# Performance work log

Measured on AMD Instinct MI355X. Metric: run time of the kernel, lower is better.

Reference implementation:

```python
import jax, jax.numpy as jnp
import numpy as np

# gen_dx_bx([-30,30,0.15], [-15,15,0.15])
DX = jnp.array([0.15, 0.15], dtype=jnp.float32)
BX = jnp.array([-29.925, -14.925], dtype=jnp.float32)


def _pairwise_dist(a, b):
    # torch.cdist p=2: [Na,2] x [Nb,2] -> [Na,Nb]
    return jnp.sqrt(jnp.sum((a[:, None, :] - b[None, :, :]) ** 2, axis=-1))


def _single(match, position, semantic, pts, ins, typ):
    # match [M,M] (M=N+1 with dustbin), position [N,2], semantic [C,N],
    # pts [G,2], ins [G] int, typ [G] int. Assumes mask is all-ones (set in setup_inputs).
    N = position.shape[0]
    M = match.shape[0]
    G = pts.shape[0]
    C = semantic.shape[0]

    pos = position * DX + BX                      # grid -> meters
    cd = _pairwise_dist(pos, pts)                 # [N,G]
    nearest = cd.argmin(-1).astype(jnp.int32)     # [N]
    cdist_mean = jnp.mean(cd.min(-1))             # mean of per-pred nearest-GT distance
    dist_map = _pairwise_dist(pos, pos)           # [N,N]
    nmax = nearest.max()

    # precompute, for every gt index g, whether any pred maps to it and the
    # closest such pred (torch: idx_pred_next[cdist[idx_pred_next, g].argmin()])
    assign = nearest[:, None] == jnp.arange(G, dtype=jnp.int32)[None, :]  # [N,G]
    exists_g = assign.any(0)                                              # [G]
    best_pred_g = jnp.where(assign, cd, jnp.inf).argmin(0).astype(jnp.int32)  # [G]

    def walk(start_gt):
        # greedy forward walk along gt indices; replicates the python while-loop,
        # including torch's negative-index wrap (idx % G) for idx_gt_next = -1.
        def cond(st):
            return ~st[2]

        def body(st):
            idx, steps, done, res = st
            is_end = idx >= nmax
            g_next_raw = jnp.where(is_end, jnp.int32(-1), idx + 1)
            g_next = jnp.mod(g_next_raw, G)
            ex = (~is_end) & exists_g[g_next]  # nearest==-1 never holds in torch
            same = ins[jnp.mod(idx, G)] == ins[g_next]
            matched = ex & same
            stop = matched | (~same) | (steps >= G + 2)  # safety bound
            res_new = jnp.where(matched, best_pred_g[g_next], jnp.int32(-1))
            return (g_next_raw, steps + jnp.int32(1), stop, res_new)

        st = (start_gt, jnp.int32(0), jnp.bool_(False), jnp.int32(-1))
        return jax.lax.while_loop(cond, body, st)[3]

    next_pred = jax.vmap(walk)(nearest)  # [N], -1 means no match (dustbin later)

    # build match_gt [M,M]
    A = jnp.zeros((M, M), dtype=match.dtype)
    valid = next_pred >= 0
    cols = jnp.where(valid, next_pred, 0)
    A = A.at[jnp.arange(N), cols].max(valid.astype(match.dtype))

    # resolve columns matched by multiple rows: keep the row closest in dist_map
    Acols = A[:, :N]
    col_sum = Acols.sum(0)
    dist_pad = jnp.concatenate([dist_map, jnp.full((1, N), jnp.inf, dist_map.dtype)], 0)  # [M,N]
    keep = jnp.where(Acols > 0, dist_pad, jnp.inf).argmin(0)  # [N]
    onehot = (jnp.arange(M)[:, None] == keep[None, :]).astype(match.dtype)
    Acols = jnp.where(col_sum[None, :] > 1, onehot, Acols)
    A = A.at[:, :N].set(Acols)

    # unmatched pred rows -> dustbin column; unmatched pred cols -> dustbin row
    row_sum = A[:N].sum(1)
    A = A.at[:N, M - 1].set(jnp.where(row_sum == 0, 1.0, A[:N, M - 1]))
    col_sum2 = A[:, :N].sum(0)
    A = A.at[M - 1, :N].set(jnp.where(col_sum2 == 0, 1.0, A[M - 1, :N]))

    # semantic gt: one-hot of the type of each pred's nearest gt point
    cls = typ[nearest]  # [N]
    semantic_gt = (jnp.arange(C)[:, None] == cls[None, :]).astype(semantic.dtype)  # [C,N]

    # NLL match loss (torch transposes then feeds NLLLoss: loss = -match[j, target[j]])
    tgt_b = A.argmax(0)  # per-column gt row
    tgt_f = A.argmax(1)  # per-row gt col
    j = jnp.arange(M - 1)
    loss_b = -jnp.mean(match[j, tgt_b[: M - 1]])
    loss_f = -jnp.mean(match[j, tgt_f[: M - 1]])
    match_loss = 0.5 * (loss_f + loss_b)

    sem_loss = -jnp.mean(semantic[semantic_gt.argmax(0), jnp.arange(N)])
    return cdist_mean, match_loss, sem_loss, A, semantic_gt


def setup_inputs() -> dict:
    key = jax.random.key(0)
    ks = jax.random.split(key, 5)
    B, N, G, C, NI = 4, 2048, 1024, 3, 32
    # log-probability score matrix with dustbin (Sinkhorn-style output)
    matches = jax.nn.log_softmax(jax.random.normal(ks[0], (B, N + 1, N + 1), jnp.float32), axis=-1)
    # predicted vertex grid coords on the 400x200 BEV grid
    positions = jax.random.uniform(ks[1], (B, N, 2), jnp.float32) * jnp.array([400.0, 200.0], jnp.float32)
    semantics = jax.nn.log_softmax(jax.random.normal(ks[2], (B, C, N), jnp.float32), axis=1)
    masks = jnp.ones((B, N, 1), jnp.float32)
    # gt points in meters within the BEV range
    gt_pts = (jax.random.uniform(ks[3], (B, G, 2), jnp.float32) - 0.5) * jnp.array([60.0, 30.0], jnp.float32)
    # sorted instance ids -> contiguous runs like the original per-instance list build
    gt_ins = jnp.sort(jax.random.randint(ks[4], (B, G), 0, NI), axis=-1).astype(jnp.int32)
    gt_type = (gt_ins % C).astype(jnp.int32)
    return {"matches": matches, "positions": positions, "semantics": semantics,
            "masks": masks, "gt_pts": gt_pts, "gt_ins": gt_ins, "gt_type": gt_type}


def reference(matches, positions, semantics, masks, gt_pts, gt_ins, gt_type):
    cm, ml, sl, mg, sg = jax.vmap(_single)(matches, positions, semantics, gt_pts, gt_ins, gt_type)
    # reduction='mean'
    return jnp.mean(cm), jnp.mean(ml), jnp.mean(sl), mg, sg
```

## Files before the change

kernel.cpp:

```cpp
#include <hip/hip_runtime.h>
#include <math.h>

#define BB 4
#define NN 2048
#define GG 1024
#define CC 3
#define MM 2049
#define SP 8
#define CH (GG / SP)

typedef unsigned long long u64;
#define KEY_EMPTY 0xFFFFFFFFFFFFFFFFULL

struct Ws {
  u64   near_key[BB * NN];
  u64   best_key[BB * GG];
  u64   keep_key[BB * NN];
  int   nearest[BB * NN];
  int   next_pred[BB * NN];
  int   col_cnt[BB * NN];
  int   nmax[BB];
  float cdist_sum[BB];
  float sem_sum[BB];
  float lossf_sum[BB];
  float lossb_sum[BB];
};

__device__ __forceinline__ float posx(float p) { return __fadd_rn(__fmul_rn(p, 0.15f), -29.925f); }
__device__ __forceinline__ float posy(float p) { return __fadd_rn(__fmul_rn(p, 0.15f), -14.925f); }
__device__ __forceinline__ float pdist(float ax, float ay, float bx, float by) {
  float dx = __fsub_rn(ax, bx);
  float dy = __fsub_rn(ay, by);
  return __fsqrt_rn(__fadd_rn(__fmul_rn(dx, dx), __fmul_rn(dy, dy)));
}
__device__ __forceinline__ u64 pack_key(float d, int i) {
  return ((u64)__float_as_uint(d) << 32) | (unsigned int)i;
}


__global__ void k_init(Ws* ws) {
  int t = blockIdx.x * blockDim.x + threadIdx.x;
  if (t < BB * NN) {
    ws->near_key[t] = KEY_EMPTY;
    ws->keep_key[t] = KEY_EMPTY;
    ws->col_cnt[t] = 0;
  }
  if (t < BB * GG) ws->best_key[t] = KEY_EMPTY;
  if (t < BB) {
    ws->nmax[t] = 0;
    ws->cdist_sum[t] = 0.f;
    ws->sem_sum[t] = 0.f;
    ws->lossf_sum[t] = 0.f;
    ws->lossb_sum[t] = 0.f;
  }
}

__global__ __launch_bounds__(256) void k_near1(const float* __restrict__ positions,
                                               const float* __restrict__ gt_pts, Ws* ws) {
  __shared__ float spts[CH * 2];
  const int cpb = NN / 256;
  int b = blockIdx.x / (cpb * SP);
  int r = blockIdx.x % (cpb * SP);
  int i = (r / SP) * 256 + threadIdx.x;
  int g0 = (r % SP) * CH;

  spts[threadIdx.x] = gt_pts[b * GG * 2 + g0 * 2 + threadIdx.x];
  __syncthreads();

  float px = posx(positions[(size_t)(b * NN + i) * 2 + 0]);
  float py = posy(positions[(size_t)(b * NN + i) * 2 + 1]);

  float dmin = INFINITY;
  int gmin = 0;
  #pragma unroll 4
  for (int g = 0; g < CH; ++g) {
    float d = pdist(px, py, spts[2 * g], spts[2 * g + 1]);
    if (d < dmin) { dmin = d; gmin = g; }
  }
  atomicMin(&ws->near_key[b * NN + i], pack_key(dmin, g0 + gmin));
}

__global__ __launch_bounds__(64) void k_near2(const int* __restrict__ gt_type,
                                              const float* __restrict__ semantics,
                                              Ws* ws, float* __restrict__ out) {
  int b = blockIdx.x >> 5;
  int i = (blockIdx.x & 31) * 64 + threadIdx.x;

  u64 key = ws->near_key[b * NN + i];
  float dmin = __uint_as_float((unsigned int)(key >> 32));
  int g = (int)(key & 0xFFFFFFFFULL);

  ws->nearest[b * NN + i] = g;
  atomicMin(&ws->best_key[b * GG + g], pack_key(dmin, i));

  int cls = gt_type[b * GG + g];
  float* sg = out + 3 + (size_t)BB * MM * MM;
  sg[(size_t)b * CC * NN + 0 * NN + i] = (cls == 0) ? 1.f : 0.f;
  sg[(size_t)b * CC * NN + 1 * NN + i] = (cls == 1) ? 1.f : 0.f;
  sg[(size_t)b * CC * NN + 2 * NN + i] = (cls == 2) ? 1.f : 0.f;
  float sem = semantics[(size_t)b * CC * NN + (size_t)cls * NN + i];

  float v = dmin;
  #pragma unroll
  for (int o = 32; o > 0; o >>= 1) v += __shfl_down(v, o, 64);
  if (threadIdx.x == 0) atomicAdd(&ws->cdist_sum[b], v);

  v = sem;
  #pragma unroll
  for (int o = 32; o > 0; o >>= 1) v += __shfl_down(v, o, 64);
  if (threadIdx.x == 0) atomicAdd(&ws->sem_sum[b], v);

  int m = g;
  #pragma unroll
  for (int o = 32; o > 0; o >>= 1) m = max(m, __shfl_down(m, o, 64));
  if (threadIdx.x == 0) atomicMax(&ws->nmax[b], m);
}

__global__ __launch_bounds__(64) void k_walk(const int* __restrict__ gt_ins,
                                             const float* __restrict__ positions, Ws* ws) {
  __shared__ int sins[GG];
  __shared__ int sbest[GG];
  int b = blockIdx.x >> 5;
  int i = (blockIdx.x & 31) * 64 + threadIdx.x;

  {
    const int4* src = reinterpret_cast<const int4*>(gt_ins + b * GG);
    int4* dst = reinterpret_cast<int4*>(sins);
    for (int t = threadIdx.x; t < GG / 4; t += 64) dst[t] = src[t];
    const u64* bk = ws->best_key + b * GG;
    for (int t = threadIdx.x; t < GG; t += 64) {
      u64 k = bk[t];
      sbest[t] = (k == KEY_EMPTY) ? -1 : (int)(k & 0xFFFFFFFFULL);
    }
  }
  __syncthreads();

  int nmax = ws->nmax[b];
  int idx = ws->nearest[b * NN + i];
  int steps = 0, res = -1;
  while (true) {
    bool is_end = idx >= nmax;
    int gnr = is_end ? -1 : idx + 1;
    int gn = gnr & (GG - 1);
    bool ex = (!is_end) && (sbest[gn] >= 0);
    bool same = sins[idx & (GG - 1)] == sins[gn];
    bool matched = ex && same;
    res = matched ? sbest[gn] : -1;
    bool stop = matched || (!same) || (steps >= GG + 2);
    idx = gnr;
    ++steps;
    if (stop) break;
  }
  ws->next_pred[b * NN + i] = res;
  if (res >= 0) {
    atomicAdd(&ws->col_cnt[b * NN + res], 1);
    const float* pb = positions + (size_t)b * NN * 2;
    float d = pdist(posx(pb[2 * i]), posy(pb[2 * i + 1]),
                    posx(pb[2 * res]), posy(pb[2 * res + 1]));
    atomicMin(&ws->keep_key[b * NN + res], pack_key(d, i));
  }
}

__global__ __launch_bounds__(64) void k_post(const float* __restrict__ matches,
                                             Ws* ws, float* __restrict__ out) {
  int b = blockIdx.x >> 5;
  int i = (blockIdx.x & 31) * 64 + threadIdx.x;

  float* A = out + 3 + (size_t)b * MM * MM;

  int j = ws->next_pred[b * NN + i];
  bool surv = (j >= 0) && ((int)(ws->keep_key[b * NN + j] & 0xFFFFFFFFULL) == i);
  if (surv) A[(size_t)i * MM + j] = 1.0f;
  else      A[(size_t)i * MM + (MM - 1)] = 1.0f;

  int cnt = ws->col_cnt[b * NN + i];
  if (cnt == 0) A[(size_t)(MM - 1) * MM + i] = 1.0f;

  int tf = surv ? j : (MM - 1);
  float vf = matches[(size_t)b * MM * MM + (size_t)i * MM + tf];
  int tb = (cnt > 0) ? (int)(ws->keep_key[b * NN + i] & 0xFFFFFFFFULL) : (MM - 1);
  float vb = matches[(size_t)b * MM * MM + (size_t)i * MM + tb];

  float v = vf;
  #pragma unroll
  for (int o = 32; o > 0; o >>= 1) v += __shfl_down(v, o, 64);
  if (threadIdx.x == 0) atomicAdd(&ws->lossf_sum[b], v);

  v = vb;
  #pragma unroll
  for (int o = 32; o > 0; o >>= 1) v += __shfl_down(v, o, 64);
  if (threadIdx.x == 0) atomicAdd(&ws->lossb_sum[b], v);
}

__global__ void k_final(Ws* ws, float* __restrict__ out) {
  if (threadIdx.x == 0 && blockIdx.x == 0) {
    float cm = 0.f, ml = 0.f, sl = 0.f;
    for (int b = 0; b < BB; ++b) {
      cm += ws->cdist_sum[b] / (float)NN;
      float lf = -(ws->lossf_sum[b] / (float)(MM - 1));
      float lb = -(ws->lossb_sum[b] / (float)(MM - 1));
      ml += 0.5f * (lf + lb);
      sl += -(ws->sem_sum[b] / (float)NN);
    }
    out[0] = cm / (float)BB;
    out[1] = ml / (float)BB;
    out[2] = sl / (float)BB;
  }
}

extern "C" void kernel_launch(void* const* d_in, const int* in_sizes, int n_in,
                              void* d_out, int out_size, void* d_ws, size_t ws_size,
                              hipStream_t stream) {
  (void)in_sizes; (void)n_in; (void)ws_size;
  const float* matches   = (const float*)d_in[0];
  const float* positions = (const float*)d_in[1];
  const float* semantics = (const float*)d_in[2];
  const float* gt_pts    = (const float*)d_in[4];
  const int*   gt_ins    = (const int*)d_in[5];
  const int*   gt_type   = (const int*)d_in[6];
  float* out = (float*)d_out;
  Ws* ws = (Ws*)d_ws;

  hipMemsetAsync(d_out, 0, (size_t)out_size * sizeof(float), stream);
  k_init<<<(BB * NN + 255) / 256, 256, 0, stream>>>(ws);
  k_near1<<<BB * (NN / 256) * SP, 256, 0, stream>>>(positions, gt_pts, ws);
  k_near2<<<BB * (NN / 64), 64, 0, stream>>>(gt_type, semantics, ws, out);
  k_walk<<<BB * (NN / 64), 64, 0, stream>>>(gt_ins, positions, ws);
  k_post<<<BB * (NN / 64), 64, 0, stream>>>(matches, ws, out);
  k_final<<<1, 64, 0, stream>>>(ws, out);
}
```

Before: 150.8 us.

## Fuse all stages into one cooperative kernel with grid syncs

```diff
diff --git a/kernel.cpp b/kernel.cpp
--- a/kernel.cpp
+++ b/kernel.cpp
@@ -1,5 +1,8 @@
 #include <hip/hip_runtime.h>
+#include <hip/hip_cooperative_groups.h>
 #include <math.h>
+
+namespace cg = cooperative_groups;
 
 #define BB 4
 #define NN 2048
@@ -8,6 +11,8 @@
 #define MM 2049
 #define SP 8
 #define CH (GG / SP)
+#define NBLK 256
+#define NTHR 256
 
 typedef unsigned long long u64;
 #define KEY_EMPTY 0xFFFFFFFFFFFFFFFFULL
@@ -37,163 +42,171 @@
   return ((u64)__float_as_uint(d) << 32) | (unsigned int)i;
 }
 
-
-__global__ void k_init(Ws* ws) {
-  int t = blockIdx.x * blockDim.x + threadIdx.x;
-  if (t < BB * NN) {
-    ws->near_key[t] = KEY_EMPTY;
-    ws->keep_key[t] = KEY_EMPTY;
-    ws->col_cnt[t] = 0;
-  }
-  if (t < BB * GG) ws->best_key[t] = KEY_EMPTY;
-  if (t < BB) {
-    ws->nmax[t] = 0;
-    ws->cdist_sum[t] = 0.f;
-    ws->sem_sum[t] = 0.f;
-    ws->lossf_sum[t] = 0.f;
-    ws->lossb_sum[t] = 0.f;
-  }
-}
-
-__global__ __launch_bounds__(256) void k_near1(const float* __restrict__ positions,
-                                               const float* __restrict__ gt_pts, Ws* ws) {
-  __shared__ float spts[CH * 2];
-  const int cpb = NN / 256;
-  int b = blockIdx.x / (cpb * SP);
-  int r = blockIdx.x % (cpb * SP);
-  int i = (r / SP) * 256 + threadIdx.x;
-  int g0 = (r % SP) * CH;
-
-  spts[threadIdx.x] = gt_pts[b * GG * 2 + g0 * 2 + threadIdx.x];
-  __syncthreads();
-
-  float px = posx(positions[(size_t)(b * NN + i) * 2 + 0]);
-  float py = posy(positions[(size_t)(b * NN + i) * 2 + 1]);
-
-  float dmin = INFINITY;
-  int gmin = 0;
-  #pragma unroll 4
-  for (int g = 0; g < CH; ++g) {
-    float d = pdist(px, py, spts[2 * g], spts[2 * g + 1]);
-    if (d < dmin) { dmin = d; gmin = g; }
-  }
-  atomicMin(&ws->near_key[b * NN + i], pack_key(dmin, g0 + gmin));
-}
-
-__global__ __launch_bounds__(64) void k_near2(const int* __restrict__ gt_type,
+__global__ __launch_bounds__(NTHR) void k_all(const float* __restrict__ matches,
+                                              const float* __restrict__ positions,
                                               const float* __restrict__ semantics,
-                                              Ws* ws, float* __restrict__ out) {
-  int b = blockIdx.x >> 5;
-  int i = (blockIdx.x & 31) * 64 + threadIdx.x;
-
-  u64 key = ws->near_key[b * NN + i];
-  float dmin = __uint_as_float((unsigned int)(key >> 32));
-  int g = (int)(key & 0xFFFFFFFFULL);
-
-  ws->nearest[b * NN + i] = g;
-  atomicMin(&ws->best_key[b * GG + g], pack_key(dmin, i));
-
-  int cls = gt_type[b * GG + g];
-  float* sg = out + 3 + (size_t)BB * MM * MM;
-  sg[(size_t)b * CC * NN + 0 * NN + i] = (cls == 0) ? 1.f : 0.f;
-  sg[(size_t)b * CC * NN + 1 * NN + i] = (cls == 1) ? 1.f : 0.f;
-  sg[(size_t)b * CC * NN + 2 * NN + i] = (cls == 2) ? 1.f : 0.f;
-  float sem = semantics[(size_t)b * CC * NN + (size_t)cls * NN + i];
-
-  float v = dmin;
-  #pragma unroll
-  for (int o = 32; o > 0; o >>= 1) v += __shfl_down(v, o, 64);
-  if (threadIdx.x == 0) atomicAdd(&ws->cdist_sum[b], v);
-
-  v = sem;
-  #pragma unroll
-  for (int o = 32; o > 0; o >>= 1) v += __shfl_down(v, o, 64);
-  if (threadIdx.x == 0) atomicAdd(&ws->sem_sum[b], v);
-
-  int m = g;
-  #pragma unroll
-  for (int o = 32; o > 0; o >>= 1) m = max(m, __shfl_down(m, o, 64));
-  if (threadIdx.x == 0) atomicMax(&ws->nmax[b], m);
-}
-
-__global__ __launch_bounds__(64) void k_walk(const int* __restrict__ gt_ins,
-                                             const float* __restrict__ positions, Ws* ws) {
-  __shared__ int sins[GG];
-  __shared__ int sbest[GG];
-  int b = blockIdx.x >> 5;
-  int i = (blockIdx.x & 31) * 64 + threadIdx.x;
+                                              const float* __restrict__ gt_pts,
+                                              const int* __restrict__ gt_ins,
+                                              const int* __restrict__ gt_type,
+                                              Ws* ws, float* __restrict__ out, int out_size) {
+  cg::grid_group grid = cg::this_grid();
+  __shared__ int smem[2 * GG];
+  const int bid = blockIdx.x, tid = threadIdx.x;
+  const int gtid = bid * NTHR + tid;
+  const int NT = NBLK * NTHR;
 
   {
-    const int4* src = reinterpret_cast<const int4*>(gt_ins + b * GG);
-    int4* dst = reinterpret_cast<int4*>(sins);
-    for (int t = threadIdx.x; t < GG / 4; t += 64) dst[t] = src[t];
-    const u64* bk = ws->best_key + b * GG;
-    for (int t = threadIdx.x; t < GG; t += 64) {
-      u64 k = bk[t];
+    int n4 = out_size >> 2;
+    float4 z = make_float4(0.f, 0.f, 0.f, 0.f);
+    float4* o4 = reinterpret_cast<float4*>(out);
+    for (int t = gtid; t < n4; t += NT) o4[t] = z;
+    if (gtid < (out_size & 3)) out[n4 * 4 + gtid] = 0.f;
+    if (gtid < BB * NN) {
+      ws->near_key[gtid] = KEY_EMPTY;
+      ws->keep_key[gtid] = KEY_EMPTY;
+      ws->col_cnt[gtid] = 0;
+    }
+    if (gtid < BB * GG) ws->best_key[gtid] = KEY_EMPTY;
+    if (gtid < BB) {
+      ws->nmax[gtid] = 0;
+      ws->cdist_sum[gtid] = 0.f;
+      ws->sem_sum[gtid] = 0.f;
+      ws->lossf_sum[gtid] = 0.f;
+      ws->lossb_sum[gtid] = 0.f;
+    }
+  }
+  grid.sync();
+
+  {
+    int b = bid >> 6;
+    int r = bid & 63;
+    int i = (r >> 3) * NTHR + tid;
+    int g0 = (r & 7) * CH;
+    float* spts = reinterpret_cast<float*>(smem);
+    spts[tid] = gt_pts[b * GG * 2 + g0 * 2 + tid];
+    __syncthreads();
+
+    float px = posx(positions[(size_t)(b * NN + i) * 2 + 0]);
+    float py = posy(positions[(size_t)(b * NN + i) * 2 + 1]);
+
+    float dmin = INFINITY;
+    int gmin = 0;
+    #pragma unroll 4
+    for (int g = 0; g < CH; ++g) {
+      float d = pdist(px, py, spts[2 * g], spts[2 * g + 1]);
+      if (d < dmin) { dmin = d; gmin = g; }
+    }
+    atomicMin(&ws->near_key[b * NN + i], pack_key(dmin, g0 + gmin));
+  }
+  grid.sync();
+
+  if (bid < 128 && tid < 64) {
+    int w = bid * 64 + tid;
+    int b = w >> 11, i = w & (NN - 1);
+
+    u64 key = ws->near_key[b * NN + i];
+    float dmin = __uint_as_float((unsigned int)(key >> 32));
+    int g = (int)(key & 0xFFFFFFFFULL);
+
+    ws->nearest[b * NN + i] = g;
+    atomicMin(&ws->best_key[b * GG + g], pack_key(dmin, i));
+
+    int cls = gt_type[b * GG + g];
+    float* sg = out + 3 + (size_t)BB * MM * MM;
+    sg[(size_t)b * CC * NN + 0 * NN + i] = (cls == 0) ? 1.f : 0.f;
+    sg[(size_t)b * CC * NN + 1 * NN + i] = (cls == 1) ? 1.f : 0.f;
+    sg[(size_t)b * CC * NN + 2 * NN + i] = (cls == 2) ? 1.f : 0.f;
+    float sem = semantics[(size_t)b * CC * NN + (size_t)cls * NN + i];
+
+    float v = dmin;
+    #pragma unroll
+    for (int o = 32; o > 0; o >>= 1) v += __shfl_down(v, o, 64);
+    if (tid == 0) atomicAdd(&ws->cdist_sum[b], v);
+
+    v = sem;
+    #pragma unroll
+    for (int o = 32; o > 0; o >>= 1) v += __shfl_down(v, o, 64);
+    if (tid == 0) atomicAdd(&ws->sem_sum[b], v);
+
+    int m = g;
+    #pragma unroll
+    for (int o = 32; o > 0; o >>= 1) m = max(m, __shfl_down(m, o, 64));
+    if (tid == 0) atomicMax(&ws->nmax[b], m);
+  }
+  grid.sync();
+
+  if (bid < 32) {
+    int w = bid * NTHR + tid;
+    int b = w >> 11, i = w & (NN - 1);
+    int* sins = smem;
+    int* sbest = smem + GG;
+
+    for (int t = tid; t < GG; t += NTHR) {
+      sins[t] = gt_ins[b * GG + t];
+      u64 k = ws->best_key[b * GG + t];
       sbest[t] = (k == KEY_EMPTY) ? -1 : (int)(k & 0xFFFFFFFFULL);
     }
-  }
-  __syncthreads();
-
-  int nmax = ws->nmax[b];
-  int idx = ws->nearest[b * NN + i];
-  int steps = 0, res = -1;
-  while (true) {
-    bool is_end = idx >= nmax;
-    int gnr = is_end ? -1 : idx + 1;
-    int gn = gnr & (GG - 1);
-    bool ex = (!is_end) && (sbest[gn] >= 0);
-    bool same = sins[idx & (GG - 1)] == sins[gn];
-    bool matched = ex && same;
-    res = matched ? sbest[gn] : -1;
-    bool stop = matched || (!same) || (steps >= GG + 2);
-    idx = gnr;
-    ++steps;
-    if (stop) break;
-  }
-  ws->next_pred[b * NN + i] = res;
-  if (res >= 0) {
-    atomicAdd(&ws->col_cnt[b * NN + res], 1);
-    const float* pb = positions + (size_t)b * NN * 2;
-    float d = pdist(posx(pb[2 * i]), posy(pb[2 * i + 1]),
-                    posx(pb[2 * res]), posy(pb[2 * res + 1]));
-    atomicMin(&ws->keep_key[b * NN + res], pack_key(d, i));
-  }
-}
-
-__global__ __launch_bounds__(64) void k_post(const float* __restrict__ matches,
-                                             Ws* ws, float* __restrict__ out) {
-  int b = blockIdx.x >> 5;
-  int i = (blockIdx.x & 31) * 64 + threadIdx.x;
-
-  float* A = out + 3 + (size_t)b * MM * MM;
-
-  int j = ws->next_pred[b * NN + i];
-  bool surv = (j >= 0) && ((int)(ws->keep_key[b * NN + j] & 0xFFFFFFFFULL) == i);
-  if (surv) A[(size_t)i * MM + j] = 1.0f;
-  else      A[(size_t)i * MM + (MM - 1)] = 1.0f;
-
-  int cnt = ws->col_cnt[b * NN + i];
-  if (cnt == 0) A[(size_t)(MM - 1) * MM + i] = 1.0f;
-
-  int tf = surv ? j : (MM - 1);
-  float vf = matches[(size_t)b * MM * MM + (size_t)i * MM + tf];
-  int tb = (cnt > 0) ? (int)(ws->keep_key[b * NN + i] & 0xFFFFFFFFULL) : (MM - 1);
-  float vb = matches[(size_t)b * MM * MM + (size_t)i * MM + tb];
-
-  float v = vf;
-  #pragma unroll
-  for (int o = 32; o > 0; o >>= 1) v += __shfl_down(v, o, 64);
-  if (threadIdx.x == 0) atomicAdd(&ws->lossf_sum[b], v);
-
-  v = vb;
-  #pragma unroll
-  for (int o = 32; o > 0; o >>= 1) v += __shfl_down(v, o, 64);
-  if (threadIdx.x == 0) atomicAdd(&ws->lossb_sum[b], v);
-}
-
-__global__ void k_final(Ws* ws, float* __restrict__ out) {
-  if (threadIdx.x == 0 && blockIdx.x == 0) {
+    __syncthreads();
+
+    int nmax = ws->nmax[b];
+    int idx = ws->nearest[b * NN + i];
+    int steps = 0, res = -1;
+    while (true) {
+      bool is_end = idx >= nmax;
+      int gnr = is_end ? -1 : idx + 1;
+      int gn = gnr & (GG - 1);
+      bool ex = (!is_end) && (sbest[gn] >= 0);
+      bool same = sins[idx & (GG - 1)] == sins[gn];
+      bool matched = ex && same;
+      res = matched ? sbest[gn] : -1;
+      bool stop = matched || (!same) || (steps >= GG + 2);
+      idx = gnr;
+      ++steps;
+      if (stop) break;
+    }
+    ws->next_pred[b * NN + i] = res;
+    if (res >= 0) {
+      atomicAdd(&ws->col_cnt[b * NN + res], 1);
+      const float* pb = positions + (size_t)b * NN * 2;
+      float d = pdist(posx(pb[2 * i]), posy(pb[2 * i + 1]),
+                      posx(pb[2 * res]), posy(pb[2 * res + 1]));
+      atomicMin(&ws->keep_key[b * NN + res], pack_key(d, i));
+    }
+  }
+  grid.sync();
+
+  if (bid < 128 && tid < 64) {
+    int w = bid * 64 + tid;
+    int b = w >> 11, i = w & (NN - 1);
+
+    float* A = out + 3 + (size_t)b * MM * MM;
+
+    int j = ws->next_pred[b * NN + i];
+    bool surv = (j >= 0) && ((int)(ws->keep_key[b * NN + j] & 0xFFFFFFFFULL) == i);
+    if (surv) A[(size_t)i * MM + j] = 1.0f;
+    else      A[(size_t)i * MM + (MM - 1)] = 1.0f;
+
+    int cnt = ws->col_cnt[b * NN + i];
+    if (cnt == 0) A[(size_t)(MM - 1) * MM + i] = 1.0f;
+
+    int tf = surv ? j : (MM - 1);
+    float vf = matches[(size_t)b * MM * MM + (size_t)i * MM + tf];
+    int tb = (cnt > 0) ? (int)(ws->keep_key[b * NN + i] & 0xFFFFFFFFULL) : (MM - 1);
+    float vb = matches[(size_t)b * MM * MM + (size_t)i * MM + tb];
+
+    float v = vf;
+    #pragma unroll
+    for (int o = 32; o > 0; o >>= 1) v += __shfl_down(v, o, 64);
+    if (tid == 0) atomicAdd(&ws->lossf_sum[b], v);
+
+    v = vb;
+    #pragma unroll
+    for (int o = 32; o > 0; o >>= 1) v += __shfl_down(v, o, 64);
+    if (tid == 0) atomicAdd(&ws->lossb_sum[b], v);
+  }
+  grid.sync();
+
+  if (gtid == 0) {
     float cm = 0.f, ml = 0.f, sl = 0.f;
     for (int b = 0; b < BB; ++b) {
       cm += ws->cdist_sum[b] / (float)NN;
@@ -220,12 +233,10 @@
   const int*   gt_type   = (const int*)d_in[6];
   float* out = (float*)d_out;
   Ws* ws = (Ws*)d_ws;
-
-  hipMemsetAsync(d_out, 0, (size_t)out_size * sizeof(float), stream);
-  k_init<<<(BB * NN + 255) / 256, 256, 0, stream>>>(ws);
-  k_near1<<<BB * (NN / 256) * SP, 256, 0, stream>>>(positions, gt_pts, ws);
-  k_near2<<<BB * (NN / 64), 64, 0, stream>>>(gt_type, semantics, ws, out);
-  k_walk<<<BB * (NN / 64), 64, 0, stream>>>(gt_ins, positions, ws);
-  k_post<<<BB * (NN / 64), 64, 0, stream>>>(matches, ws, out);
-  k_final<<<1, 64, 0, stream>>>(ws, out);
-}
+  int osz = out_size;
+
+  void* args[] = {(void*)&matches, (void*)&positions, (void*)&semantics,
+                  (void*)&gt_pts, (void*)&gt_ins, (void*)&gt_type,
+                  (void*)&ws, (void*)&out, (void*)&osz};
+  hipLaunchCooperativeKernel((const void*)k_all, dim3(NBLK), dim3(NTHR), args, 0, stream);
+}
```

Result: slower. 286.9 us (+90.3%).
